# Optimization experiments

Hardware: AMD Instinct MI355X
Metric: run time of the kernel (lower is better)

Reference implementation:

```python
import jax, jax.numpy as jnp
import numpy as np

N_NODES = 100000

def _sage_conv(x, edge_index, W_l, b_l, W_r):
    # PyG SAGEConv default: mean-aggregate neighbor (source) features at dst,
    # then out = lin_l(agg) + lin_r(x). lin_l has bias, lin_r does not.
    src, dst = edge_index[0], edge_index[1]
    msg = x[src]                                   # [E, F]
    summed = jax.ops.segment_sum(msg, dst, num_segments=N_NODES)  # [N, F]
    cnt = jax.ops.segment_sum(jnp.ones((src.shape[0],), x.dtype), dst,
                              num_segments=N_NODES)
    agg = summed / jnp.maximum(cnt, 1.0)[:, None]
    return agg @ W_l + b_l + x @ W_r


def setup_inputs() -> dict:
    key = jax.random.key(0)
    ks = jax.random.split(key, 10)
    F_IN, H, C = 128, 16, 8
    E = 3200000
    x = jax.random.normal(ks[0], (N_NODES, F_IN), dtype=jnp.float32)
    edge_index = jax.random.randint(ks[1], (2, E), 0, N_NODES, dtype=jnp.int64)
    s1 = 1.0 / np.sqrt(F_IN)
    s2 = 1.0 / np.sqrt(H)
    sc = 1.0 / np.sqrt(2 * H)
    return {
        "x": x,
        "edge_index": edge_index,
        "W1_l": jax.random.uniform(ks[2], (F_IN, H), jnp.float32, -s1, s1),
        "b1": jnp.zeros((H,), jnp.float32),
        "W1_r": jax.random.uniform(ks[3], (F_IN, H), jnp.float32, -s1, s1),
        "W2_l": jax.random.uniform(ks[4], (H, H), jnp.float32, -s2, s2),
        "b2": jnp.zeros((H,), jnp.float32),
        "W2_r": jax.random.uniform(ks[5], (H, H), jnp.float32, -s2, s2),
        "Wc": jax.random.uniform(ks[6], (2 * H, C), jnp.float32, -sc, sc),
        "bc": jax.random.uniform(ks[7], (C,), jnp.float32, -sc, sc),
    }


def reference(x, edge_index, W1_l, b1, W1_r, W2_l, b2, W2_r, Wc, bc):
    h = jax.nn.relu(_sage_conv(x, edge_index, W1_l, b1, W1_r))
    # F.dropout(training=False) in eval mode -> identity
    h = jax.nn.relu(_sage_conv(h, edge_index, W2_l, b2, W2_r))
    edge_feat = jnp.concatenate([h[edge_index[0]], h[edge_index[1]]], axis=-1)  # [E, 32]
    logits = edge_feat @ Wc + bc                                                # [E, C]
    return jax.nn.log_softmax(logits, axis=1)
```

## Files before the change

### kernel.cpp

```cpp
#include <hip/hip_runtime.h>
#include <hip/hip_bf16.h>
#include <hip/hip_fp16.h>


#define NBLK 512
#define BUCKET_BITS 9
#define BUCKET_SZ 512
#define MAXNB 256
#define STAGE_CAP 36000

struct __align__(16) H8 { __half2 a, b, c, d; };

__global__ __launch_bounds__(512) void bincount_kernel(const int* __restrict__ ei,
                                                       int* __restrict__ counts,
                                                       int E, int NB, int chunk) {
  __shared__ int hist[MAXNB];
  for (int i = threadIdx.x; i < NB; i += 512) hist[i] = 0;
  __syncthreads();
  int s = blockIdx.x * chunk;
  int eend = s + chunk; if (eend > E) eend = E;
  for (int e = s + threadIdx.x; e < eend; e += 512)
    atomicAdd(&hist[ei[E + e] >> BUCKET_BITS], 1);
  __syncthreads();
  for (int b = threadIdx.x; b < NB; b += 512)
    counts[b * NBLK + blockIdx.x] = hist[b];
}

__global__ __launch_bounds__(512) void scan1_kernel(const int* __restrict__ counts,
                                                    int* __restrict__ locoff,
                                                    int* __restrict__ total) {
  __shared__ int wsum[8];
  int b = blockIdx.x;
  int t = threadIdx.x;
  int lane = t & 63, wid = t >> 6;
  int v = counts[b * NBLK + t];
  int incl = v;
#pragma unroll
  for (int d = 1; d < 64; d <<= 1) {
    int u = __shfl_up(incl, d);
    if (lane >= d) incl += u;
  }
  if (lane == 63) wsum[wid] = incl;
  __syncthreads();
  if (t < 64) {
    int w = (t < 8) ? wsum[t] : 0;
#pragma unroll
    for (int d = 1; d < 8; d <<= 1) {
      int u = __shfl_up(w, d);
      if (lane >= d) w += u;
    }
    if (t < 8) wsum[t] = w;
  }
  __syncthreads();
  int excl = ((wid > 0) ? wsum[wid - 1] : 0) + (incl - v);
  locoff[b * NBLK + t] = excl;
  if (t == NBLK - 1) total[b] = excl + v;
}

__global__ __launch_bounds__(256) void scan2_kernel(const int* __restrict__ total,
                                                    int* __restrict__ bstart, int NB) {
  __shared__ int wsum[4];
  int t = threadIdx.x;
  int lane = t & 63, wid = t >> 6;
  int v = (t < NB) ? total[t] : 0;
  int incl = v;
#pragma unroll
  for (int d = 1; d < 64; d <<= 1) {
    int u = __shfl_up(incl, d);
    if (lane >= d) incl += u;
  }
  if (lane == 63) wsum[wid] = incl;
  __syncthreads();
  if (t < 64) {
    int w = (t < 4) ? wsum[t] : 0;
#pragma unroll
    for (int d = 1; d < 4; d <<= 1) {
      int u = __shfl_up(w, d);
      if (lane >= d) w += u;
    }
    if (t < 4) wsum[t] = w;
  }
  __syncthreads();
  int excl = ((wid > 0) ? wsum[wid - 1] : 0) + (incl - v);
  if (t <= NB) bstart[t] = excl;
}

__global__ __launch_bounds__(512) void binwrite_kernel(const int* __restrict__ ei,
                                                       const int* __restrict__ locoff,
                                                       const int* __restrict__ bstart,
                                                       int* __restrict__ elist,
                                                       int E, int NB, int chunk) {
  __shared__ int cur[MAXNB];
  for (int b = threadIdx.x; b < NB; b += 512)
    cur[b] = bstart[b] + locoff[b * NBLK + blockIdx.x];
  __syncthreads();
  int s = blockIdx.x * chunk;
  int eend = s + chunk; if (eend > E) eend = E;
  for (int e = s + threadIdx.x; e < eend; e += 512) {
    int src = ei[e];
    int dst = ei[E + e];
    int b = dst >> BUCKET_BITS;
    int pos = atomicAdd(&cur[b], 1);
    elist[pos] = ((dst & (BUCKET_SZ - 1)) << 17) | src;
  }
}

__global__ __launch_bounds__(1024) void sort_kernel(int* __restrict__ elist,
                                                    const int* __restrict__ bstart,
                                                    int* __restrict__ row_csr,
                                                    int N) {
  extern __shared__ int sm[];
  int* stage = sm;
  int* hist  = sm + STAGE_CAP;
  int* wtmp  = hist + 512;
  int t = threadIdx.x;
  int b = blockIdx.x;
  int beg = bstart[b];
  int end = bstart[b + 1];
  int cnt = end - beg;
  if (cnt > STAGE_CAP) cnt = STAGE_CAP;
  for (int i = t; i < cnt; i += 1024) stage[i] = elist[beg + i];
  if (t < 512) hist[t] = 0;
  __syncthreads();
  for (int i = t; i < cnt; i += 1024)
    atomicAdd(&hist[((unsigned)stage[i]) >> 17], 1);
  __syncthreads();
  int lane = t & 63;
  int wv = t >> 6;
  int v = (t < 512) ? hist[t] : 0;
  int incl = v;
#pragma unroll
  for (int d = 1; d < 64; d <<= 1) {
    int u = __shfl_up(incl, d);
    if (lane >= d) incl += u;
  }
  if (t < 512 && lane == 63) wtmp[wv] = incl;
  __syncthreads();
  if (t < 64) {
    int w = (t < 8) ? wtmp[t] : 0;
#pragma unroll
    for (int d = 1; d < 8; d <<= 1) {
      int u = __shfl_up(w, d);
      if (lane >= d) w += u;
    }
    if (t < 8) wtmp[t] = w;
  }
  __syncthreads();
  if (t < 512) {
    int excl = ((wv > 0) ? wtmp[wv - 1] : 0) + (incl - v);
    hist[t] = excl;
    int node = (b << BUCKET_BITS) + t;
    if (node <= N) row_csr[node] = beg + excl;
  }
  __syncthreads();
  for (int i = t; i < cnt; i += 1024) {
    unsigned ent = (unsigned)stage[i];
    int pos = atomicAdd(&hist[ent >> 17], 1);
    elist[beg + pos] = ent & 0x1FFFF;
  }
}

__global__ __launch_bounds__(256) void lin1_kernel(const float* __restrict__ x,
                                                   const float* __restrict__ W1l,
                                                   const float* __restrict__ W1r,
                                                   __half* __restrict__ yh,
                                                   float* __restrict__ z, int N) {
  __shared__ float Xs[32 * 129];
  __shared__ float Ws[128 * 32];
  int t = threadIdx.x;
  for (int i = t; i < 128 * 16; i += 256) {
    int k = i >> 4, c = i & 15;
    Ws[k * 32 + c] = W1l[i];
    Ws[k * 32 + 16 + c] = W1r[i];
  }
  int nb = blockIdx.x * 32;
  const float4* xg = (const float4*)(x + (size_t)nb * 128);
  for (int i4 = t; i4 < 32 * 32; i4 += 256) {
    float4 val = xg[i4];
    int r = i4 >> 5, c4 = (i4 & 31) * 4;
    float* dp = &Xs[r * 129 + c4];
    dp[0] = val.x; dp[1] = val.y; dp[2] = val.z; dp[3] = val.w;
  }
  __syncthreads();
  int n = t & 31, cg = t >> 5;
  float a0 = 0.f, a1 = 0.f, a2 = 0.f, a3 = 0.f;
  for (int k = 0; k < 128; ++k) {
    float xv = Xs[n * 129 + k];
    const float* wr = &Ws[k * 32 + cg * 4];
    a0 += xv * wr[0]; a1 += xv * wr[1]; a2 += xv * wr[2]; a3 += xv * wr[3];
  }
  int node = nb + n;
  if (node < N) {
    int c = cg * 4;
    if (c < 16) {
      __half2* yp = (__half2*)(yh + (size_t)node * 16 + c);
      yp[0] = __floats2half2_rn(a0, a1);
      yp[1] = __floats2half2_rn(a2, a3);
    } else {
      float* op = z + (size_t)node * 16 + (c - 16);
      op[0] = a0; op[1] = a1; op[2] = a2; op[3] = a3;
    }
  }
}

__global__ __launch_bounds__(256) void agg1_kernel(const __half* __restrict__ yh,
                                                   const float* __restrict__ z,
                                                   const int* __restrict__ row_csr,
                                                   const int* __restrict__ srclist,
                                                   const float* __restrict__ b1,
                                                   const float* __restrict__ W2l,
                                                   const float* __restrict__ W2r,
                                                   __half* __restrict__ ph,
                                                   float* __restrict__ q, int N) {
  int g = (blockIdx.x * 256 + threadIdx.x) >> 4;
  int k = threadIdx.x & 15;
  if (g >= N) return;
  int beg = row_csr[g], end = row_csr[g + 1];
  float acc = 0.f;
  int j = beg;
  for (; j + 4 <= end; j += 4) {
    int s0 = srclist[j], s1 = srclist[j + 1];
    int s2 = srclist[j + 2], s3 = srclist[j + 3];
    acc += __half2float(yh[(size_t)s0 * 16 + k]);
    acc += __half2float(yh[(size_t)s1 * 16 + k]);
    acc += __half2float(yh[(size_t)s2 * 16 + k]);
    acc += __half2float(yh[(size_t)s3 * 16 + k]);
  }
  for (; j < end; ++j) acc += __half2float(yh[(size_t)srclist[j] * 16 + k]);
  int deg = end - beg;
  float mean = acc / (float)(deg > 0 ? deg : 1);
  float h = fmaxf(mean + b1[k] + z[(size_t)g * 16 + k], 0.f);
  float pa = 0.f, qa = 0.f;
#pragma unroll
  for (int kk = 0; kk < 16; ++kk) {
    float hk = __shfl(h, kk, 16);
    pa += hk * W2l[kk * 16 + k];
    qa += hk * W2r[kk * 16 + k];
  }
  ph[(size_t)g * 16 + k] = __float2half(pa);
  q[(size_t)g * 16 + k] = qa;
}

__global__ __launch_bounds__(256) void agg2_kernel(const __half* __restrict__ ph,
                                                   const float* __restrict__ q,
                                                   const int* __restrict__ row_csr,
                                                   const int* __restrict__ srclist,
                                                   const float* __restrict__ b2,
                                                   const float* __restrict__ Wc,
                                                   __half* __restrict__ Uh,
                                                   __half* __restrict__ Vh, int N) {
  int g = (blockIdx.x * 256 + threadIdx.x) >> 4;
  int k = threadIdx.x & 15;
  if (g >= N) return;
  int beg = row_csr[g], end = row_csr[g + 1];
  float acc = 0.f;
  int j = beg;
  for (; j + 4 <= end; j += 4) {
    int s0 = srclist[j], s1 = srclist[j + 1];
    int s2 = srclist[j + 2], s3 = srclist[j + 3];
    acc += __half2float(ph[(size_t)s0 * 16 + k]);
    acc += __half2float(ph[(size_t)s1 * 16 + k]);
    acc += __half2float(ph[(size_t)s2 * 16 + k]);
    acc += __half2float(ph[(size_t)s3 * 16 + k]);
  }
  for (; j < end; ++j) acc += __half2float(ph[(size_t)srclist[j] * 16 + k]);
  int deg = end - beg;
  float mean = acc / (float)(deg > 0 ? deg : 1);
  float h = fmaxf(mean + b2[k] + q[(size_t)g * 16 + k], 0.f);
  int wbase = (k < 8) ? 0 : 16;
  int c = k & 7;
  float o = 0.f;
#pragma unroll
  for (int kk = 0; kk < 16; ++kk) {
    float hk = __shfl(h, kk, 16);
    o += hk * Wc[(wbase + kk) * 8 + c];
  }
  if (k < 8) Uh[(size_t)g * 8 + c] = __float2half(o);
  else       Vh[(size_t)g * 8 + c] = __float2half(o);
}

__global__ __launch_bounds__(256) void edge_out_kernel(const int* __restrict__ ei,
                                                       const __half* __restrict__ Uh,
                                                       const __half* __restrict__ Vh,
                                                       const float* __restrict__ bc,
                                                       float* __restrict__ out, int E) {
  int e = blockIdx.x * 256 + threadIdx.x;
  if (e >= E) return;
  int src = ei[e];
  int dst = ei[E + e];
  H8 u8 = *(const H8*)(Uh + (size_t)src * 8);
  H8 v8 = *(const H8*)(Vh + (size_t)dst * 8);
  float4 c0 = ((const float4*)bc)[0], c1 = ((const float4*)bc)[1];
  float2 ua = __half22float2(u8.a), ub = __half22float2(u8.b);
  float2 uc = __half22float2(u8.c), ud = __half22float2(u8.d);
  float2 va = __half22float2(v8.a), vb = __half22float2(v8.b);
  float2 vc = __half22float2(v8.c), vd = __half22float2(v8.d);
  float t[8];
  t[0] = ua.x + va.x + c0.x; t[1] = ua.y + va.y + c0.y;
  t[2] = ub.x + vb.x + c0.z; t[3] = ub.y + vb.y + c0.w;
  t[4] = uc.x + vc.x + c1.x; t[5] = uc.y + vc.y + c1.y;
  t[6] = ud.x + vd.x + c1.z; t[7] = ud.y + vd.y + c1.w;
  float m = t[0];
#pragma unroll
  for (int c = 1; c < 8; ++c) m = fmaxf(m, t[c]);
  float s = 0.f;
#pragma unroll
  for (int c = 0; c < 8; ++c) s += __expf(t[c] - m);
  float lse = m + __logf(s);
  float4 o0 = make_float4(t[0] - lse, t[1] - lse, t[2] - lse, t[3] - lse);
  float4 o1 = make_float4(t[4] - lse, t[5] - lse, t[6] - lse, t[7] - lse);
  float4* op = (float4*)(out + (size_t)e * 8);
  op[0] = o0; op[1] = o1;
}

extern "C" void kernel_launch(void* const* d_in, const int* in_sizes, int n_in,
                              void* d_out, int out_size, void* d_ws, size_t ws_size,
                              hipStream_t stream) {
  const float* x   = (const float*)d_in[0];
  const int*   ei  = (const int*)d_in[1];
  const float* W1l = (const float*)d_in[2];
  const float* b1  = (const float*)d_in[3];
  const float* W1r = (const float*)d_in[4];
  const float* W2l = (const float*)d_in[5];
  const float* b2  = (const float*)d_in[6];
  const float* W2r = (const float*)d_in[7];
  const float* Wc  = (const float*)d_in[8];
  const float* bc  = (const float*)d_in[9];
  float* out = (float*)d_out;

  const int N = in_sizes[0] / 128;
  const int E = in_sizes[1] / 2;
  const size_t N16 = (size_t)N * 16;
  const int NB = (N + BUCKET_SZ - 1) >> BUCKET_BITS;
  const int chunk = (E + NBLK - 1) / NBLK;

  __half* yh = (__half*)d_ws;
  __half* ph = yh + N16;
  __half* Uh = ph + N16;
  __half* Vh = Uh + (size_t)N * 8;
  float*  z  = (float*)(Vh + (size_t)N * 8);
  float*  q  = z + N16;
  int* counts  = (int*)(q + N16);
  int* locoff  = counts + NB * NBLK;
  int* total   = locoff + NB * NBLK;
  int* bstart  = total + NB;
  int* elist   = bstart + NB + 1;
  int* row_csr = elist + E;

  bincount_kernel<<<NBLK, 512, 0, stream>>>(ei, counts, E, NB, chunk);
  scan1_kernel<<<NB, 512, 0, stream>>>(counts, locoff, total);
  scan2_kernel<<<1, 256, 0, stream>>>(total, bstart, NB);
  binwrite_kernel<<<NBLK, 512, 0, stream>>>(ei, locoff, bstart, elist, E, NB, chunk);
  size_t smem = (STAGE_CAP + 512 + 16) * sizeof(int);
  sort_kernel<<<NB, 1024, smem, stream>>>(elist, bstart, row_csr, N);

  lin1_kernel<<<(N + 31) / 32, 256, 0, stream>>>(x, W1l, W1r, yh, z, N);

  int ngrid = (N * 16 + 255) / 256;
  agg1_kernel<<<ngrid, 256, 0, stream>>>(yh, z, row_csr, elist, b1, W2l, W2r, ph, q, N);
  agg2_kernel<<<ngrid, 256, 0, stream>>>(ph, q, row_csr, elist, b2, Wc, Uh, Vh, N);

  int egrid = (E + 255) / 256;
  edge_out_kernel<<<egrid, 256, 0, stream>>>(ei, Uh, Vh, bc, out, E);
}
```

Measured before the change: 211.1 us.

## Fuse bincount with lin1, fold scan2 into consumers, vectorize aggregation and edge output

Merges the edge bincount and the first linear layer into one heterogeneous launch, and removes the separate scan2 kernel by recomputing the bucket prefix sum inside binwrite and sort. The aggregation kernels now use 8 lanes per node reading half2 pairs, with weights staged in shared memory. The edge output kernel handles 4 edges per thread with vector nontemporal index loads. Together these cut launch count, redundant scalar loads and per-edge index traffic, at the cost of repeated small scans in every block and more registers per thread.

```diff
diff --git a/kernel.cpp b/kernel.cpp
--- a/kernel.cpp
+++ b/kernel.cpp
@@ -10,20 +10,68 @@
 #define STAGE_CAP 36000
 
 struct __align__(16) H8 { __half2 a, b, c, d; };
-
-__global__ __launch_bounds__(512) void bincount_kernel(const int* __restrict__ ei,
-                                                       int* __restrict__ counts,
-                                                       int E, int NB, int chunk) {
-  __shared__ int hist[MAXNB];
-  for (int i = threadIdx.x; i < NB; i += 512) hist[i] = 0;
-  __syncthreads();
-  int s = blockIdx.x * chunk;
-  int eend = s + chunk; if (eend > E) eend = E;
-  for (int e = s + threadIdx.x; e < eend; e += 512)
-    atomicAdd(&hist[ei[E + e] >> BUCKET_BITS], 1);
-  __syncthreads();
-  for (int b = threadIdx.x; b < NB; b += 512)
-    counts[b * NBLK + blockIdx.x] = hist[b];
+typedef int i32x4 __attribute__((ext_vector_type(4)));
+
+__global__ __launch_bounds__(512) void prep_kernel(const int* __restrict__ ei,
+                                                   int* __restrict__ counts,
+                                                   const float* __restrict__ x,
+                                                   const float* __restrict__ W1l,
+                                                   const float* __restrict__ W1r,
+                                                   __half* __restrict__ yh,
+                                                   float* __restrict__ z,
+                                                   int E, int N, int NB, int chunk,
+                                                   int nbin) {
+  __shared__ float smem[64 * 129 + 128 * 32];
+  int t = threadIdx.x;
+  if ((int)blockIdx.x < nbin) {
+    int* hist = (int*)smem;
+    for (int i = t; i < NB; i += 512) hist[i] = 0;
+    __syncthreads();
+    int s = blockIdx.x * chunk;
+    int eend = s + chunk; if (eend > E) eend = E;
+    for (int e = s + t; e < eend; e += 512)
+      atomicAdd(&hist[ei[E + e] >> BUCKET_BITS], 1);
+    __syncthreads();
+    for (int b = t; b < NB; b += 512)
+      counts[b * NBLK + blockIdx.x] = hist[b];
+  } else {
+    float* Xs = smem;
+    float* Ws = smem + 64 * 129;
+    int nb = ((int)blockIdx.x - nbin) * 64;
+    for (int i = t; i < 128 * 16; i += 512) {
+      int kk = i >> 4, c = i & 15;
+      Ws[kk * 32 + c] = W1l[i];
+      Ws[kk * 32 + 16 + c] = W1r[i];
+    }
+    const float4* xg = (const float4*)(x + (size_t)nb * 128);
+    for (int i4 = t; i4 < 64 * 32; i4 += 512) {
+      int r = i4 >> 5, c4 = (i4 & 31) * 4;
+      float4 val = make_float4(0.f, 0.f, 0.f, 0.f);
+      if (nb + r < N) val = xg[i4];
+      float* dp = &Xs[r * 129 + c4];
+      dp[0] = val.x; dp[1] = val.y; dp[2] = val.z; dp[3] = val.w;
+    }
+    __syncthreads();
+    int n = t & 63, cg = t >> 6;
+    float a0 = 0.f, a1 = 0.f, a2 = 0.f, a3 = 0.f;
+    for (int kk = 0; kk < 128; ++kk) {
+      float xv = Xs[n * 129 + kk];
+      const float* wr = &Ws[kk * 32 + cg * 4];
+      a0 += xv * wr[0]; a1 += xv * wr[1]; a2 += xv * wr[2]; a3 += xv * wr[3];
+    }
+    int node = nb + n;
+    if (node < N) {
+      int c = cg * 4;
+      if (c < 16) {
+        __half2* yp = (__half2*)(yh + (size_t)node * 16 + c);
+        yp[0] = __floats2half2_rn(a0, a1);
+        yp[1] = __floats2half2_rn(a2, a3);
+      } else {
+        float* op = z + (size_t)node * 16 + (c - 16);
+        op[0] = a0; op[1] = a1; op[2] = a2; op[3] = a3;
+      }
+    }
+  }
 }
 
 __global__ __launch_bounds__(512) void scan1_kernel(const int* __restrict__ counts,
@@ -57,46 +105,40 @@
   if (t == NBLK - 1) total[b] = excl + v;
 }
 
-__global__ __launch_bounds__(256) void scan2_kernel(const int* __restrict__ total,
-                                                    int* __restrict__ bstart, int NB) {
-  __shared__ int wsum[4];
+__global__ __launch_bounds__(512) void binwrite_kernel(const int* __restrict__ ei,
+                                                       const int* __restrict__ locoff,
+                                                       const int* __restrict__ total,
+                                                       int* __restrict__ elist,
+                                                       int E, int NB, int chunk) {
+  __shared__ int cur[MAXNB];
+  __shared__ int ws4[4];
   int t = threadIdx.x;
   int lane = t & 63, wid = t >> 6;
-  int v = (t < NB) ? total[t] : 0;
+  int v = (t < 256 && t < NB) ? total[t] : 0;
   int incl = v;
 #pragma unroll
   for (int d = 1; d < 64; d <<= 1) {
     int u = __shfl_up(incl, d);
     if (lane >= d) incl += u;
   }
-  if (lane == 63) wsum[wid] = incl;
+  if (t < 256 && lane == 63) ws4[wid] = incl;
   __syncthreads();
   if (t < 64) {
-    int w = (t < 4) ? wsum[t] : 0;
+    int w = (t < 4) ? ws4[t] : 0;
 #pragma unroll
     for (int d = 1; d < 4; d <<= 1) {
       int u = __shfl_up(w, d);
       if (lane >= d) w += u;
     }
-    if (t < 4) wsum[t] = w;
-  }
-  __syncthreads();
-  int excl = ((wid > 0) ? wsum[wid - 1] : 0) + (incl - v);
-  if (t <= NB) bstart[t] = excl;
-}
-
-__global__ __launch_bounds__(512) void binwrite_kernel(const int* __restrict__ ei,
-                                                       const int* __restrict__ locoff,
-                                                       const int* __restrict__ bstart,
-                                                       int* __restrict__ elist,
-                                                       int E, int NB, int chunk) {
-  __shared__ int cur[MAXNB];
-  for (int b = threadIdx.x; b < NB; b += 512)
-    cur[b] = bstart[b] + locoff[b * NBLK + blockIdx.x];
+    if (t < 4) ws4[t] = w;
+  }
+  __syncthreads();
+  if (t < 256 && t < NB)
+    cur[t] = ((wid > 0) ? ws4[wid - 1] : 0) + (incl - v) + locoff[t * NBLK + blockIdx.x];
   __syncthreads();
   int s = blockIdx.x * chunk;
   int eend = s + chunk; if (eend > E) eend = E;
-  for (int e = s + threadIdx.x; e < eend; e += 512) {
+  for (int e = s + t; e < eend; e += 512) {
     int src = ei[e];
     int dst = ei[E + e];
     int b = dst >> BUCKET_BITS;
@@ -106,18 +148,42 @@
 }
 
 __global__ __launch_bounds__(1024) void sort_kernel(int* __restrict__ elist,
-                                                    const int* __restrict__ bstart,
+                                                    const int* __restrict__ total,
                                                     int* __restrict__ row_csr,
-                                                    int N) {
+                                                    int N, int NB) {
   extern __shared__ int sm[];
   int* stage = sm;
   int* hist  = sm + STAGE_CAP;
   int* wtmp  = hist + 512;
+  __shared__ int beg_s;
   int t = threadIdx.x;
   int b = blockIdx.x;
-  int beg = bstart[b];
-  int end = bstart[b + 1];
-  int cnt = end - beg;
+  int lane = t & 63, wid = t >> 6;
+  {
+    int v = (t < 256 && t < NB) ? total[t] : 0;
+    int incl = v;
+#pragma unroll
+    for (int d = 1; d < 64; d <<= 1) {
+      int u = __shfl_up(incl, d);
+      if (lane >= d) incl += u;
+    }
+    if (t < 256 && lane == 63) wtmp[wid] = incl;
+    __syncthreads();
+    if (t < 64) {
+      int w = (t < 4) ? wtmp[t] : 0;
+#pragma unroll
+      for (int d = 1; d < 4; d <<= 1) {
+        int u = __shfl_up(w, d);
+        if (lane >= d) w += u;
+      }
+      if (t < 4) wtmp[t] = w;
+    }
+    __syncthreads();
+    if (t == b) beg_s = ((wid > 0) ? wtmp[wid - 1] : 0) + (incl - v);
+    __syncthreads();
+  }
+  int beg = beg_s;
+  int cnt = total[b];
   if (cnt > STAGE_CAP) cnt = STAGE_CAP;
   for (int i = t; i < cnt; i += 1024) stage[i] = elist[beg + i];
   if (t < 512) hist[t] = 0;
@@ -125,8 +191,6 @@
   for (int i = t; i < cnt; i += 1024)
     atomicAdd(&hist[((unsigned)stage[i]) >> 17], 1);
   __syncthreads();
-  int lane = t & 63;
-  int wv = t >> 6;
   int v = (t < 512) ? hist[t] : 0;
   int incl = v;
 #pragma unroll
@@ -134,7 +198,7 @@
     int u = __shfl_up(incl, d);
     if (lane >= d) incl += u;
   }
-  if (t < 512 && lane == 63) wtmp[wv] = incl;
+  if (t < 512 && lane == 63) wtmp[wid] = incl;
   __syncthreads();
   if (t < 64) {
     int w = (t < 8) ? wtmp[t] : 0;
@@ -147,7 +211,7 @@
   }
   __syncthreads();
   if (t < 512) {
-    int excl = ((wv > 0) ? wtmp[wv - 1] : 0) + (incl - v);
+    int excl = ((wid > 0) ? wtmp[wid - 1] : 0) + (incl - v);
     hist[t] = excl;
     int node = (b << BUCKET_BITS) + t;
     if (node <= N) row_csr[node] = beg + excl;
@@ -157,49 +221,6 @@
     unsigned ent = (unsigned)stage[i];
     int pos = atomicAdd(&hist[ent >> 17], 1);
     elist[beg + pos] = ent & 0x1FFFF;
-  }
-}
-
-__global__ __launch_bounds__(256) void lin1_kernel(const float* __restrict__ x,
-                                                   const float* __restrict__ W1l,
-                                                   const float* __restrict__ W1r,
-                                                   __half* __restrict__ yh,
-                                                   float* __restrict__ z, int N) {
-  __shared__ float Xs[32 * 129];
-  __shared__ float Ws[128 * 32];
-  int t = threadIdx.x;
-  for (int i = t; i < 128 * 16; i += 256) {
-    int k = i >> 4, c = i & 15;
-    Ws[k * 32 + c] = W1l[i];
-    Ws[k * 32 + 16 + c] = W1r[i];
-  }
-  int nb = blockIdx.x * 32;
-  const float4* xg = (const float4*)(x + (size_t)nb * 128);
-  for (int i4 = t; i4 < 32 * 32; i4 += 256) {
-    float4 val = xg[i4];
-    int r = i4 >> 5, c4 = (i4 & 31) * 4;
-    float* dp = &Xs[r * 129 + c4];
-    dp[0] = val.x; dp[1] = val.y; dp[2] = val.z; dp[3] = val.w;
-  }
-  __syncthreads();
-  int n = t & 31, cg = t >> 5;
-  float a0 = 0.f, a1 = 0.f, a2 = 0.f, a3 = 0.f;
-  for (int k = 0; k < 128; ++k) {
-    float xv = Xs[n * 129 + k];
-    const float* wr = &Ws[k * 32 + cg * 4];
-    a0 += xv * wr[0]; a1 += xv * wr[1]; a2 += xv * wr[2]; a3 += xv * wr[3];
-  }
-  int node = nb + n;
-  if (node < N) {
-    int c = cg * 4;
-    if (c < 16) {
-      __half2* yp = (__half2*)(yh + (size_t)node * 16 + c);
-      yp[0] = __floats2half2_rn(a0, a1);
-      yp[1] = __floats2half2_rn(a2, a3);
-    } else {
-      float* op = z + (size_t)node * 16 + (c - 16);
-      op[0] = a0; op[1] = a1; op[2] = a2; op[3] = a3;
-    }
   }
 }
 
@@ -212,33 +233,51 @@
                                                    const float* __restrict__ W2r,
                                                    __half* __restrict__ ph,
                                                    float* __restrict__ q, int N) {
-  int g = (blockIdx.x * 256 + threadIdx.x) >> 4;
-  int k = threadIdx.x & 15;
+  __shared__ float Wl_s[256], Wr_s[256], b_s[16];
+  int t = threadIdx.x;
+  if (t < 256) { Wl_s[t] = W2l[t]; Wr_s[t] = W2r[t]; }
+  if (t < 16) b_s[t] = b1[t];
+  __syncthreads();
+  int g = (blockIdx.x * 256 + t) >> 3;
+  int k = t & 7;
   if (g >= N) return;
   int beg = row_csr[g], end = row_csr[g + 1];
-  float acc = 0.f;
+  const __half2* yh2 = (const __half2*)yh;
+  float a0 = 0.f, a1 = 0.f;
   int j = beg;
   for (; j + 4 <= end; j += 4) {
     int s0 = srclist[j], s1 = srclist[j + 1];
     int s2 = srclist[j + 2], s3 = srclist[j + 3];
-    acc += __half2float(yh[(size_t)s0 * 16 + k]);
-    acc += __half2float(yh[(size_t)s1 * 16 + k]);
-    acc += __half2float(yh[(size_t)s2 * 16 + k]);
-    acc += __half2float(yh[(size_t)s3 * 16 + k]);
-  }
-  for (; j < end; ++j) acc += __half2float(yh[(size_t)srclist[j] * 16 + k]);
+    float2 v0 = __half22float2(yh2[(size_t)s0 * 8 + k]);
+    float2 v1 = __half22float2(yh2[(size_t)s1 * 8 + k]);
+    float2 v2 = __half22float2(yh2[(size_t)s2 * 8 + k]);
+    float2 v3 = __half22float2(yh2[(size_t)s3 * 8 + k]);
+    a0 += v0.x + v1.x + v2.x + v3.x;
+    a1 += v0.y + v1.y + v2.y + v3.y;
+  }
+  for (; j < end; ++j) {
+    float2 v = __half22float2(yh2[(size_t)srclist[j] * 8 + k]);
+    a0 += v.x; a1 += v.y;
+  }
   int deg = end - beg;
-  float mean = acc / (float)(deg > 0 ? deg : 1);
-  float h = fmaxf(mean + b1[k] + z[(size_t)g * 16 + k], 0.f);
-  float pa = 0.f, qa = 0.f;
-#pragma unroll
-  for (int kk = 0; kk < 16; ++kk) {
-    float hk = __shfl(h, kk, 16);
-    pa += hk * W2l[kk * 16 + k];
-    qa += hk * W2r[kk * 16 + k];
-  }
-  ph[(size_t)g * 16 + k] = __float2half(pa);
-  q[(size_t)g * 16 + k] = qa;
+  float inv = 1.f / (float)(deg > 0 ? deg : 1);
+  float2 zv = ((const float2*)z)[(size_t)g * 8 + k];
+  float h0 = fmaxf(a0 * inv + b_s[2 * k]     + zv.x, 0.f);
+  float h1 = fmaxf(a1 * inv + b_s[2 * k + 1] + zv.y, 0.f);
+  float pa0 = 0.f, pa1 = 0.f, qa0 = 0.f, qa1 = 0.f;
+  int c0 = 2 * k;
+#pragma unroll
+  for (int kk2 = 0; kk2 < 8; ++kk2) {
+    float ha = __shfl(h0, kk2, 8);
+    float hb = __shfl(h1, kk2, 8);
+    int r0 = 2 * kk2 * 16, r1 = r0 + 16;
+    pa0 += ha * Wl_s[r0 + c0]     + hb * Wl_s[r1 + c0];
+    pa1 += ha * Wl_s[r0 + c0 + 1] + hb * Wl_s[r1 + c0 + 1];
+    qa0 += ha * Wr_s[r0 + c0]     + hb * Wr_s[r1 + c0];
+    qa1 += ha * Wr_s[r0 + c0 + 1] + hb * Wr_s[r1 + c0 + 1];
+  }
+  ((__half2*)ph)[(size_t)g * 8 + k] = __floats2half2_rn(pa0, pa1);
+  ((float2*)q)[(size_t)g * 8 + k] = make_float2(qa0, qa1);
 }
 
 __global__ __launch_bounds__(256) void agg2_kernel(const __half* __restrict__ ph,
@@ -249,34 +288,51 @@
                                                    const float* __restrict__ Wc,
                                                    __half* __restrict__ Uh,
                                                    __half* __restrict__ Vh, int N) {
-  int g = (blockIdx.x * 256 + threadIdx.x) >> 4;
-  int k = threadIdx.x & 15;
+  __shared__ float Wc_s[256], b_s[16];
+  int t = threadIdx.x;
+  if (t < 256) Wc_s[t] = Wc[t];
+  if (t < 16) b_s[t] = b2[t];
+  __syncthreads();
+  int g = (blockIdx.x * 256 + t) >> 3;
+  int k = t & 7;
   if (g >= N) return;
   int beg = row_csr[g], end = row_csr[g + 1];
-  float acc = 0.f;
+  const __half2* ph2 = (const __half2*)ph;
+  float a0 = 0.f, a1 = 0.f;
   int j = beg;
   for (; j + 4 <= end; j += 4) {
     int s0 = srclist[j], s1 = srclist[j + 1];
     int s2 = srclist[j + 2], s3 = srclist[j + 3];
-    acc += __half2float(ph[(size_t)s0 * 16 + k]);
-    acc += __half2float(ph[(size_t)s1 * 16 + k]);
-    acc += __half2float(ph[(size_t)s2 * 16 + k]);
-    acc += __half2float(ph[(size_t)s3 * 16 + k]);
-  }
-  for (; j < end; ++j) acc += __half2float(ph[(size_t)srclist[j] * 16 + k]);
+    float2 v0 = __half22float2(ph2[(size_t)s0 * 8 + k]);
+    float2 v1 = __half22float2(ph2[(size_t)s1 * 8 + k]);
+    float2 v2 = __half22float2(ph2[(size_t)s2 * 8 + k]);
+    float2 v3 = __half22float2(ph2[(size_t)s3 * 8 + k]);
+    a0 += v0.x + v1.x + v2.x + v3.x;
+    a1 += v0.y + v1.y + v2.y + v3.y;
+  }
+  for (; j < end; ++j) {
+    float2 v = __half22float2(ph2[(size_t)srclist[j] * 8 + k]);
+    a0 += v.x; a1 += v.y;
+  }
   int deg = end - beg;
-  float mean = acc / (float)(deg > 0 ? deg : 1);
-  float h = fmaxf(mean + b2[k] + q[(size_t)g * 16 + k], 0.f);
-  int wbase = (k < 8) ? 0 : 16;
-  int c = k & 7;
-  float o = 0.f;
-#pragma unroll
-  for (int kk = 0; kk < 16; ++kk) {
-    float hk = __shfl(h, kk, 16);
-    o += hk * Wc[(wbase + kk) * 8 + c];
-  }
-  if (k < 8) Uh[(size_t)g * 8 + c] = __float2half(o);
-  else       Vh[(size_t)g * 8 + c] = __float2half(o);
+  float inv = 1.f / (float)(deg > 0 ? deg : 1);
+  float2 qv = ((const float2*)q)[(size_t)g * 8 + k];
+  float h0 = fmaxf(a0 * inv + b_s[2 * k]     + qv.x, 0.f);
+  float h1 = fmaxf(a1 * inv + b_s[2 * k + 1] + qv.y, 0.f);
+  int wb = (k < 4) ? 0 : 128;
+  int c0 = 2 * (k & 3);
+  float o0 = 0.f, o1 = 0.f;
+#pragma unroll
+  for (int kk2 = 0; kk2 < 8; ++kk2) {
+    float ha = __shfl(h0, kk2, 8);
+    float hb = __shfl(h1, kk2, 8);
+    int r0 = wb + 2 * kk2 * 8, r1 = r0 + 8;
+    o0 += ha * Wc_s[r0 + c0]     + hb * Wc_s[r1 + c0];
+    o1 += ha * Wc_s[r0 + c0 + 1] + hb * Wc_s[r1 + c0 + 1];
+  }
+  __half2 o = __floats2half2_rn(o0, o1);
+  if (k < 4) ((__half2*)Uh)[(size_t)g * 4 + k] = o;
+  else       ((__half2*)Vh)[(size_t)g * 4 + (k - 4)] = o;
 }
 
 __global__ __launch_bounds__(256) void edge_out_kernel(const int* __restrict__ ei,
@@ -284,33 +340,52 @@
                                                        const __half* __restrict__ Vh,
                                                        const float* __restrict__ bc,
                                                        float* __restrict__ out, int E) {
-  int e = blockIdx.x * 256 + threadIdx.x;
-  if (e >= E) return;
-  int src = ei[e];
-  int dst = ei[E + e];
-  H8 u8 = *(const H8*)(Uh + (size_t)src * 8);
-  H8 v8 = *(const H8*)(Vh + (size_t)dst * 8);
+  int e0 = (blockIdx.x * 256 + threadIdx.x) * 4;
+  if (e0 >= E) return;
   float4 c0 = ((const float4*)bc)[0], c1 = ((const float4*)bc)[1];
-  float2 ua = __half22float2(u8.a), ub = __half22float2(u8.b);
-  float2 uc = __half22float2(u8.c), ud = __half22float2(u8.d);
-  float2 va = __half22float2(v8.a), vb = __half22float2(v8.b);
-  float2 vc = __half22float2(v8.c), vd = __half22float2(v8.d);
-  float t[8];
-  t[0] = ua.x + va.x + c0.x; t[1] = ua.y + va.y + c0.y;
-  t[2] = ub.x + vb.x + c0.z; t[3] = ub.y + vb.y + c0.w;
-  t[4] = uc.x + vc.x + c1.x; t[5] = uc.y + vc.y + c1.y;
-  t[6] = ud.x + vd.x + c1.z; t[7] = ud.y + vd.y + c1.w;
-  float m = t[0];
-#pragma unroll
-  for (int c = 1; c < 8; ++c) m = fmaxf(m, t[c]);
-  float s = 0.f;
-#pragma unroll
-  for (int c = 0; c < 8; ++c) s += __expf(t[c] - m);
-  float lse = m + __logf(s);
-  float4 o0 = make_float4(t[0] - lse, t[1] - lse, t[2] - lse, t[3] - lse);
-  float4 o1 = make_float4(t[4] - lse, t[5] - lse, t[6] - lse, t[7] - lse);
-  float4* op = (float4*)(out + (size_t)e * 8);
-  op[0] = o0; op[1] = o1;
+  int s[4], d[4];
+  if (e0 + 3 < E) {
+    i32x4 sv = __builtin_nontemporal_load((const i32x4*)(ei + e0));
+    i32x4 dv = __builtin_nontemporal_load((const i32x4*)(ei + E + e0));
+    s[0] = sv.x; s[1] = sv.y; s[2] = sv.z; s[3] = sv.w;
+    d[0] = dv.x; d[1] = dv.y; d[2] = dv.z; d[3] = dv.w;
+  } else {
+#pragma unroll
+    for (int ii = 0; ii < 4; ++ii) {
+      s[ii] = (e0 + ii < E) ? ei[e0 + ii] : 0;
+      d[ii] = (e0 + ii < E) ? ei[E + e0 + ii] : 0;
+    }
+  }
+  H8 u8[4], v8[4];
+#pragma unroll
+  for (int ii = 0; ii < 4; ++ii) {
+    u8[ii] = *(const H8*)(Uh + (size_t)s[ii] * 8);
+    v8[ii] = *(const H8*)(Vh + (size_t)d[ii] * 8);
+  }
+#pragma unroll
+  for (int ii = 0; ii < 4; ++ii) {
+    if (e0 + ii >= E) break;
+    float2 ua = __half22float2(u8[ii].a), ub = __half22float2(u8[ii].b);
+    float2 uc = __half22float2(u8[ii].c), ud = __half22float2(u8[ii].d);
+    float2 va = __half22float2(v8[ii].a), vb = __half22float2(v8[ii].b);
+    float2 vc = __half22float2(v8[ii].c), vd = __half22float2(v8[ii].d);
+    float tv[8];
+    tv[0] = ua.x + va.x + c0.x; tv[1] = ua.y + va.y + c0.y;
+    tv[2] = ub.x + vb.x + c0.z; tv[3] = ub.y + vb.y + c0.w;
+    tv[4] = uc.x + vc.x + c1.x; tv[5] = uc.y + vc.y + c1.y;
+    tv[6] = ud.x + vd.x + c1.z; tv[7] = ud.y + vd.y + c1.w;
+    float m = tv[0];
+#pragma unroll
+    for (int c = 1; c < 8; ++c) m = fmaxf(m, tv[c]);
+    float ssum = 0.f;
+#pragma unroll
+    for (int c = 0; c < 8; ++c) ssum += __expf(tv[c] - m);
+    float lse = m + __logf(ssum);
+    float4 o0 = make_float4(tv[0] - lse, tv[1] - lse, tv[2] - lse, tv[3] - lse);
+    float4 o1 = make_float4(tv[4] - lse, tv[5] - lse, tv[6] - lse, tv[7] - lse);
+    float4* op = (float4*)(out + (size_t)(e0 + ii) * 8);
+    op[0] = o0; op[1] = o1;
+  }
 }
 
 extern "C" void kernel_launch(void* const* d_in, const int* in_sizes, int n_in,
@@ -343,23 +418,21 @@
   int* counts  = (int*)(q + N16);
   int* locoff  = counts + NB * NBLK;
   int* total   = locoff + NB * NBLK;
-  int* bstart  = total + NB;
-  int* elist   = bstart + NB + 1;
+  int* elist   = total + NB;
   int* row_csr = elist + E;
 
-  bincount_kernel<<<NBLK, 512, 0, stream>>>(ei, counts, E, NB, chunk);
+  int lin1_blocks = (N + 63) / 64;
+  prep_kernel<<<NBLK + lin1_blocks, 512, 0, stream>>>(ei, counts, x, W1l, W1r,
+                                                      yh, z, E, N, NB, chunk, NBLK);
   scan1_kernel<<<NB, 512, 0, stream>>>(counts, locoff, total);
-  scan2_kernel<<<1, 256, 0, stream>>>(total, bstart, NB);
-  binwrite_kernel<<<NBLK, 512, 0, stream>>>(ei, locoff, bstart, elist, E, NB, chunk);
+  binwrite_kernel<<<NBLK, 512, 0, stream>>>(ei, locoff, total, elist, E, NB, chunk);
   size_t smem = (STAGE_CAP + 512 + 16) * sizeof(int);
-  sort_kernel<<<NB, 1024, smem, stream>>>(elist, bstart, row_csr, N);
-
-  lin1_kernel<<<(N + 31) / 32, 256, 0, stream>>>(x, W1l, W1r, yh, z, N);
-
-  int ngrid = (N * 16 + 255) / 256;
+  sort_kernel<<<NB, 1024, smem, stream>>>(elist, total, row_csr, N, NB);
+
+  int ngrid = (N * 8 + 255) / 256;
   agg1_kernel<<<ngrid, 256, 0, stream>>>(yh, z, row_csr, elist, b1, W2l, W2r, ph, q, N);
   agg2_kernel<<<ngrid, 256, 0, stream>>>(ph, q, row_csr, elist, b2, Wc, Uh, Vh, N);
 
-  int egrid = (E + 255) / 256;
+  int egrid = ((E + 3) / 4 + 255) / 256;
   edge_out_kernel<<<egrid, 256, 0, stream>>>(ei, Uh, Vh, bc, out, E);
 }
```

Measured after the change: 241.5 us. 1.14x slower.
